# Performance work log

Hardware: AMD Instinct MI355X
Metric: run time of the kernel (lower is better)

The kernel has to match this reference:

```python
import jax, jax.numpy as jnp
import numpy as np

FEATURE_DIM = 256
TEMP = 0.1
BASE_TEMP = 0.07
MAX_SAMPLES = 1024
SIM_THR = 0.7


def setup_inputs() -> dict:
    key = jax.random.key(0)
    ks = jax.random.split(key, 8)
    B, C, H, W = 4, FEATURE_DIM, 160, 160
    s = 1.0 / np.sqrt(C)
    return {
        'feats': jax.random.normal(ks[0], (B, C, H, W), jnp.float32),
        'labels': jax.random.randint(ks[1], (B, H, W), 0, 2).astype(jnp.int64),
        'superpixel_indice': jax.random.randint(ks[2], (B, H, W), 0, 200).astype(jnp.int64),
        'w1': jax.random.normal(ks[3], (C, C), jnp.float32) * s,
        'b1': jnp.zeros((C,), jnp.float32),
        'w2': jax.random.normal(ks[4], (C, C), jnp.float32) * s,
        'b2': jnp.zeros((C,), jnp.float32),
        'wa1': jax.random.normal(ks[5], (64, C), jnp.float32) * s,
        'ba1': jnp.zeros((64,), jnp.float32),
        'wa2': jax.random.normal(ks[6], (1, 64), jnp.float32) * (1.0 / 8.0),
        'ba2': jnp.zeros((1,), jnp.float32),
    }


def _per_sample(f, w, lab, sp):
    # f: (N, C) normalized proj feats, w: (N,) pixel weights, lab/sp: (N,) int
    valid = lab == 1
    # deterministic sample: stable-sort valid pixels to the front, take MAX_SAMPLES
    order = jnp.argsort(jnp.where(valid, 0, 1).astype(jnp.int32))
    idx = order[:MAX_SAMPLES]
    sel = valid[idx]                       # (S,) real-sample mask (pads if <S valid)
    tf = f[idx]                            # (S, C)
    tw = w[idx]                            # (S,)
    ts = sp[idx]                           # (S,)
    sim = tf @ tf.T                        # (S, S)
    S = MAX_SAMPLES
    eye = jnp.eye(S, dtype=bool)
    pos = (ts[:, None] == ts[None, :]) & (sim > SIM_THR)
    pos = pos & sel[:, None] & sel[None, :] & ~eye
    exp_sim = jnp.exp(sim / TEMP) * sel[None, :].astype(sim.dtype)
    denom = exp_sim.sum(axis=1)            # (S,)
    log_prob = sim / TEMP - jnp.log(jnp.where(denom > 0, denom, 1.0))[:, None]
    pw = tw[:, None] * tw[None, :]
    pwm = jnp.where(pos, pw, 0.0)
    psum = pwm.sum()
    loss = -(TEMP / BASE_TEMP) * (pwm * jnp.where(pos, log_prob, 0.0)).sum() / jnp.where(psum > 0, psum, 1.0)
    has = psum > 0
    return jnp.where(has, loss, 0.0), has


def reference(feats, labels, superpixel_indice, w1, b1, w2, b2, wa1, ba1, wa2, ba2):
    B, C, H, W = feats.shape
    x = jnp.transpose(feats, (0, 2, 3, 1)).reshape(B, H * W, C)  # (B, N, C)
    proj = jax.nn.relu(x @ w1.T + b1) @ w2.T + b2                # 1x1 convs == per-pixel matmul
    attn = jax.nn.sigmoid(jax.nn.relu(x @ wa1.T + ba1) @ wa2.T + ba2)[..., 0]  # (B, N)
    nrm = jnp.linalg.norm(proj, axis=-1, keepdims=True)
    fn = proj / jnp.maximum(nrm, 1e-12)
    lab = labels.reshape(B, -1)
    sp = superpixel_indice.reshape(B, -1)
    losses, flags = jax.vmap(_per_sample)(fn, attn, lab, sp)
    n = flags.sum().astype(jnp.float32)
    return jnp.where(n > 0, losses.sum() / jnp.maximum(n, 1.0), 0.0)
```

## Files before the change

kernel.cpp:

```cpp
#include <hip/hip_runtime.h>
#include <hip/hip_bf16.h>
#include <math.h>

#define NPIX   25600
#define CDIM   256
#define SSEL   1024
#define BATCH  4
#define NCHUNK 25
#define INV_T  10.0f
#define RATIO  1.4285714285714286f
#define THR    0.7f

typedef __attribute__((ext_vector_type(8))) short bf16x8;
typedef __attribute__((ext_vector_type(4))) float f32x4;

__global__ __launch_bounds__(256) void pack_weights(
    const float* __restrict__ w1, const float* __restrict__ w2,
    const float* __restrict__ wa1, const int* __restrict__ labels,
    float* __restrict__ w1p, float* __restrict__ w2p, float* __restrict__ wa1p,
    float* __restrict__ denom, float* __restrict__ Prow, float* __restrict__ Ssum,
    int* __restrict__ counts) {
  int t = threadIdx.x;
  int e = blockIdx.x * 256 + t;
  if (e < 65536) {
    int kk = e & 3;
    int c  = (e >> 2) & 255;
    int k4 = e >> 10;
    int src = c * 256 + k4 * 4 + kk;
    w1p[e] = w1[src];
    w2p[e] = w2[src];
  }
  if (e < 16384) {
    int kk = e & 3;
    int c  = (e >> 2) & 63;
    int k4 = e >> 8;
    wa1p[e] = wa1[c * 256 + k4 * 4 + kk];
  }
  if (e < BATCH * SSEL) { denom[e] = 0.f; Prow[e] = 0.f; }
  if (e < BATCH) Ssum[e] = 0.f;

  if (blockIdx.x < BATCH * NCHUNK) {
    int b = blockIdx.x / NCHUNK, ch = blockIdx.x % NCHUNK;
    const int* lab = labels + b * NPIX + ch * 1024;
    int local = 0;
#pragma unroll
    for (int q = 0; q < 4; ++q) local += (lab[q * 256 + t] == 1);
    for (int off = 32; off > 0; off >>= 1) local += __shfl_xor(local, off, 64);
    __shared__ int ws[4];
    if ((t & 63) == 0) ws[t >> 6] = local;
    __syncthreads();
    if (t == 0) counts[blockIdx.x] = ws[0] + ws[1] + ws[2] + ws[3];
  }
}

__global__ __launch_bounds__(1024) void select_scatter(
    const int* __restrict__ labels, const int* __restrict__ sp,
    const int* __restrict__ counts,
    int* __restrict__ idx, int* __restrict__ selv, int* __restrict__ tsp) {
  int b = blockIdx.x / NCHUNK, ch = blockIdx.x % NCHUNK;
  int t = threadIdx.x;
  __shared__ int cs[NCHUNK];
  __shared__ int wave_tot[16];
  if (t < NCHUNK) cs[t] = counts[b * NCHUNK + t];
  __syncthreads();
  int Vtot = 0, vbase = 0;
#pragma unroll
  for (int c = 0; c < NCHUNK; ++c) {
    int v = cs[c];
    Vtot += v;
    if (c < ch) vbase += v;
  }
  int ibase = ch * 1024 - vbase;

  int i = ch * 1024 + t;
  int isv = (labels[b * NPIX + i] == 1) ? 1 : 0;
  int lane = t & 63, wid = t >> 6;
  unsigned long long mv = __ballot(isv);
  int pv = __popcll(mv & ((1ull << lane) - 1ull));
  if (lane == 0) wave_tot[wid] = __popcll(mv);
  __syncthreads();
  for (int w = 0; w < wid; ++w) pv += wave_tot[w];
  int gslot = isv ? (vbase + pv) : (Vtot + ibase + (t - pv));
  if (gslot < SSEL) {
    idx [b * SSEL + gslot] = i;
    selv[b * SSEL + gslot] = isv;
    tsp [b * SSEL + gslot] = sp[b * NPIX + i];
  }
}

#define RROWS 16
__global__ __launch_bounds__(256) void mlp_kernel(
    const float* __restrict__ feats,
    const float* __restrict__ w1p, const float* __restrict__ b1,
    const float* __restrict__ w2p, const float* __restrict__ b2,
    const float* __restrict__ wa1p, const float* __restrict__ ba1,
    const float* __restrict__ wa2, const float* __restrict__ ba2,
    const int* __restrict__ idx,
    unsigned short* __restrict__ fnh, unsigned short* __restrict__ fnl,
    float* __restrict__ tw) {
  int r0  = blockIdx.x * RROWS;
  int b   = r0 >> 10;
  int t   = threadIdx.x;
  int lane = t & 63;

  __shared__ float xs[RROWS][256];
  __shared__ float hs[RROWS][256];
  __shared__ float apart[RROWS][64];
  __shared__ float nrm[RROWS];
  __shared__ int   ridx[RROWS];

  if (t < RROWS) { ridx[t] = idx[r0 + t]; nrm[t] = 0.f; }
  __syncthreads();

  for (int e = t; e < RROWS * 256; e += 256) {
    int r = e & 15, c = e >> 4;
    xs[r][c] = feats[((long)b * CDIM + c) * NPIX + ridx[r]];
  }
  __syncthreads();

  const float4* xs4  = reinterpret_cast<const float4*>(&xs[0][0]);
  const float4* hs4  = reinterpret_cast<const float4*>(&hs[0][0]);
  const float4* w1p4 = reinterpret_cast<const float4*>(w1p);
  const float4* w2p4 = reinterpret_cast<const float4*>(w2p);
  const float4* wa1p4= reinterpret_cast<const float4*>(wa1p);

  {
    int ca = t & 63, rg = t >> 6;
    float aacc[4] = {0.f, 0.f, 0.f, 0.f};
#pragma unroll 2
    for (int k4 = 0; k4 < 64; ++k4) {
      float4 wv = wa1p4[k4 * 64 + ca];
#pragma unroll
      for (int r = 0; r < 4; ++r) {
        float4 xv = xs4[(rg * 4 + r) * 64 + k4];
        aacc[r] += xv.x * wv.x + xv.y * wv.y + xv.z * wv.z + xv.w * wv.w;
      }
    }
    float bb = ba1[ca], w2v = wa2[ca];
#pragma unroll
    for (int r = 0; r < 4; ++r)
      apart[rg * 4 + r][ca] = fmaxf(aacc[r] + bb, 0.f) * w2v;
  }

  int c  = t & 127;
  int rg = t >> 7;
  float acc[8][2];
#pragma unroll
  for (int r = 0; r < 8; ++r) { acc[r][0] = 0.f; acc[r][1] = 0.f; }
#pragma unroll 2
  for (int k4 = 0; k4 < 64; ++k4) {
    float4 w0 = w1p4[k4 * 256 + c];
    float4 w1v = w1p4[k4 * 256 + c + 128];
#pragma unroll
    for (int r = 0; r < 8; ++r) {
      float4 xv = xs4[(rg * 8 + r) * 64 + k4];
      acc[r][0] += xv.x * w0.x + xv.y * w0.y + xv.z * w0.z + xv.w * w0.w;
      acc[r][1] += xv.x * w1v.x + xv.y * w1v.y + xv.z * w1v.z + xv.w * w1v.w;
    }
  }
  {
    float bb0 = b1[c], bb1 = b1[c + 128];
#pragma unroll
    for (int r = 0; r < 8; ++r) {
      hs[rg * 8 + r][c]       = fmaxf(acc[r][0] + bb0, 0.f);
      hs[rg * 8 + r][c + 128] = fmaxf(acc[r][1] + bb1, 0.f);
    }
  }
  __syncthreads();

#pragma unroll
  for (int r = 0; r < 8; ++r) { acc[r][0] = 0.f; acc[r][1] = 0.f; }
#pragma unroll 2
  for (int k4 = 0; k4 < 64; ++k4) {
    float4 w0 = w2p4[k4 * 256 + c];
    float4 w1v = w2p4[k4 * 256 + c + 128];
#pragma unroll
    for (int r = 0; r < 8; ++r) {
      float4 xv = hs4[(rg * 8 + r) * 64 + k4];
      acc[r][0] += xv.x * w0.x + xv.y * w0.y + xv.z * w0.z + xv.w * w0.w;
      acc[r][1] += xv.x * w1v.x + xv.y * w1v.y + xv.z * w1v.z + xv.w * w1v.w;
    }
  }
  {
    float bb0 = b2[c], bb1 = b2[c + 128];
#pragma unroll
    for (int r = 0; r < 8; ++r) { acc[r][0] += bb0; acc[r][1] += bb1; }
  }

#pragma unroll
  for (int r = 0; r < 8; ++r) {
    float v = acc[r][0] * acc[r][0] + acc[r][1] * acc[r][1];
    for (int off = 32; off > 0; off >>= 1) v += __shfl_xor(v, off, 64);
    if (lane == 0) atomicAdd(&nrm[rg * 8 + r], v);
  }
  __syncthreads();
#pragma unroll
  for (int r = 0; r < 8; ++r) {
    float den = fmaxf(sqrtf(nrm[rg * 8 + r]), 1e-12f);
    long ro = (long)(r0 + rg * 8 + r) * CDIM;
    float v0 = acc[r][0] / den;
    float v1 = acc[r][1] / den;
    __hip_bfloat16 h0 = __float2bfloat16(v0);
    __hip_bfloat16 h1 = __float2bfloat16(v1);
    __hip_bfloat16 l0 = __float2bfloat16(v0 - __bfloat162float(h0));
    __hip_bfloat16 l1 = __float2bfloat16(v1 - __bfloat162float(h1));
    fnh[ro + c]       = *reinterpret_cast<unsigned short*>(&h0);
    fnh[ro + c + 128] = *reinterpret_cast<unsigned short*>(&h1);
    fnl[ro + c]       = *reinterpret_cast<unsigned short*>(&l0);
    fnl[ro + c + 128] = *reinterpret_cast<unsigned short*>(&l1);
  }

  if (t < RROWS) {
    float s = ba2[0];
    for (int c2 = 0; c2 < 64; ++c2) s += apart[t][c2];
    tw[r0 + t] = 1.f / (1.f + expf(-s));
  }
}

__global__ __launch_bounds__(256) void sim_kernel(
    const unsigned short* __restrict__ fnh, const unsigned short* __restrict__ fnl,
    const float* __restrict__ tw,
    const int* __restrict__ selv, const int* __restrict__ tsp,
    float* __restrict__ denom, float* __restrict__ Prow, float* __restrict__ Ssum) {
  int b = blockIdx.y;
  int t = threadIdx.x;
  int lane = t & 63, w = t >> 6;
  int m = lane & 15, q = lane >> 4;

  int rem = blockIdx.x, ti = 0;
  while (rem >= (16 - ti)) { rem -= (16 - ti); ++ti; }
  int tj = ti + rem;
  bool diag = (ti == tj);
  int i0 = ti * 64, j0 = tj * 64;
  int base = b << 10;

  __shared__ __align__(16) unsigned short Ah[64 * 72], Al[64 * 72];
  __shared__ __align__(16) unsigned short Bhh[64 * 72], Bll[64 * 72];
  __shared__ float drl[64], Prl[64];
  __shared__ float dclw[4][64], Pclw[4][64];
  __shared__ float swv[4];

  const unsigned short* Bh = diag ? Ah : Bhh;
  const unsigned short* Bl = diag ? Al : Bll;

  f32x4 acc[4];
#pragma unroll
  for (int nt = 0; nt < 4; ++nt) acc[nt] = {0.f, 0.f, 0.f, 0.f};

  for (int kk = 0; kk < 4; ++kk) {
    __syncthreads();
#pragma unroll
    for (int p = 0; p < 2; ++p) {
      int e = p * 256 + t;
      int row = e >> 3, kg = e & 7;
      int lo = row * 72 + kg * 8;
      int gi_ = (base + i0 + row) * 256 + kk * 64 + kg * 8;
      *(uint4*)&Ah[lo] = *(const uint4*)&fnh[gi_];
      *(uint4*)&Al[lo] = *(const uint4*)&fnl[gi_];
      if (!diag) {
        int gj_ = (base + j0 + row) * 256 + kk * 64 + kg * 8;
        *(uint4*)&Bhh[lo] = *(const uint4*)&fnh[gj_];
        *(uint4*)&Bll[lo] = *(const uint4*)&fnl[gj_];
      }
    }
    __syncthreads();
#pragma unroll
    for (int ks = 0; ks < 2; ++ks) {
      int koff = ks * 32 + q * 8;
      int arow = w * 16 + m;
      bf16x8 ah = *(const bf16x8*)&Ah[arow * 72 + koff];
      bf16x8 al = *(const bf16x8*)&Al[arow * 72 + koff];
#pragma unroll
      for (int nt = 0; nt < 4; ++nt) {
        bf16x8 bh = *(const bf16x8*)&Bh[(nt * 16 + m) * 72 + koff];
        bf16x8 bl = *(const bf16x8*)&Bl[(nt * 16 + m) * 72 + koff];
        acc[nt] = __builtin_amdgcn_mfma_f32_16x16x32_bf16(ah, bh, acc[nt], 0, 0, 0);
        acc[nt] = __builtin_amdgcn_mfma_f32_16x16x32_bf16(ah, bl, acc[nt], 0, 0, 0);
        acc[nt] = __builtin_amdgcn_mfma_f32_16x16x32_bf16(al, bh, acc[nt], 0, 0, 0);
      }
    }
  }

  int   gi[4], gj[4], si[4], sj[4], ci[4], cj[4];
  float twi[4], twj[4];
#pragma unroll
  for (int reg = 0; reg < 4; ++reg) {
    int i = i0 + w * 16 + q * 4 + reg;
    gi[reg] = i; twi[reg] = tw[base + i];
    si[reg] = selv[base + i]; ci[reg] = tsp[base + i];
  }
#pragma unroll
  for (int nt = 0; nt < 4; ++nt) {
    int j = j0 + nt * 16 + m;
    gj[nt] = j; twj[nt] = tw[base + j];
    sj[nt] = selv[base + j]; cj[nt] = tsp[base + j];
  }

  float dR[4] = {0, 0, 0, 0}, PR[4] = {0, 0, 0, 0};
  float dC[4] = {0, 0, 0, 0}, PC[4] = {0, 0, 0, 0};
  float Sp = 0.f;
#pragma unroll
  for (int nt = 0; nt < 4; ++nt) {
#pragma unroll
    for (int reg = 0; reg < 4; ++reg) {
      float s = acc[nt][reg];
      float e10 = __expf(s * INV_T);
      if (sj[nt]) dR[reg] += e10;
      if (si[reg]) dC[nt] += e10;
      if (si[reg] && sj[nt] && (ci[reg] == cj[nt]) && (s > THR) && (gi[reg] != gj[nt])) {
        float pw = twi[reg] * twj[nt];
        PR[reg] += pw;
        PC[nt] += pw;
        Sp += pw * s;
      }
    }
  }

  for (int off = 8; off > 0; off >>= 1) {
#pragma unroll
    for (int reg = 0; reg < 4; ++reg) {
      dR[reg] += __shfl_xor(dR[reg], off, 64);
      PR[reg] += __shfl_xor(PR[reg], off, 64);
    }
  }
  if (m == 0) {
#pragma unroll
    for (int reg = 0; reg < 4; ++reg) {
      drl[w * 16 + q * 4 + reg] = dR[reg];
      Prl[w * 16 + q * 4 + reg] = PR[reg];
    }
  }
  if (!diag) {
    for (int off = 32; off >= 16; off >>= 1) {
#pragma unroll
      for (int nt = 0; nt < 4; ++nt) {
        dC[nt] += __shfl_xor(dC[nt], off, 64);
        PC[nt] += __shfl_xor(PC[nt], off, 64);
      }
    }
    if (q == 0) {
#pragma unroll
      for (int nt = 0; nt < 4; ++nt) {
        dclw[w][nt * 16 + m] = dC[nt];
        Pclw[w][nt * 16 + m] = PC[nt];
      }
    }
  }
  for (int off = 32; off > 0; off >>= 1) Sp += __shfl_xor(Sp, off, 64);
  if (lane == 0) swv[w] = Sp;
  __syncthreads();

  if (t < 64) {
    atomicAdd(&denom[base + i0 + t], drl[t]);
    atomicAdd(&Prow [base + i0 + t], Prl[t]);
    if (!diag) {
      float dc = dclw[0][t] + dclw[1][t] + dclw[2][t] + dclw[3][t];
      float pc = Pclw[0][t] + Pclw[1][t] + Pclw[2][t] + Pclw[3][t];
      atomicAdd(&denom[base + j0 + t], dc);
      atomicAdd(&Prow [base + j0 + t], pc);
    }
  }
  if (t == 0) {
    float St = swv[0] + swv[1] + swv[2] + swv[3];
    atomicAdd(&Ssum[b], diag ? St : 2.f * St);
  }
}

__global__ __launch_bounds__(1024) void finalize_kernel(
    const float* __restrict__ denom, const float* __restrict__ Prow,
    const float* __restrict__ Ssum, float* __restrict__ out) {
  int t = threadIdx.x;
  int b = t >> 8, u = t & 255;
  float P = 0.f, L = 0.f;
#pragma unroll
  for (int q = 0; q < 4; ++q) {
    int s = u + q * 256;
    float p = Prow[b * SSEL + s];
    float D = denom[b * SSEL + s];
    P += p;
    L += p * logf(D > 0.f ? D : 1.f);
  }
  for (int off = 32; off > 0; off >>= 1) {
    P += __shfl_xor(P, off, 64);
    L += __shfl_xor(L, off, 64);
  }
  __shared__ float wP[16], wL[16];
  int lane = t & 63, w = t >> 6;
  if (lane == 0) { wP[w] = P; wL[w] = L; }
  __syncthreads();
  if (t == 0) {
    float total = 0.f, n = 0.f;
    for (int bb = 0; bb < BATCH; ++bb) {
      float psum = wP[4 * bb] + wP[4 * bb + 1] + wP[4 * bb + 2] + wP[4 * bb + 3];
      float lsum = wL[4 * bb] + wL[4 * bb + 1] + wL[4 * bb + 2] + wL[4 * bb + 3];
      if (psum > 0.f) {
        float wls = Ssum[bb] * INV_T - lsum;
        total += -RATIO * wls / psum;
        n += 1.f;
      }
    }
    out[0] = (n > 0.f) ? (total / n) : 0.f;
  }
}

extern "C" void kernel_launch(void* const* d_in, const int* in_sizes, int n_in,
                              void* d_out, int out_size, void* d_ws, size_t ws_size,
                              hipStream_t stream) {
  const float* feats = (const float*)d_in[0];
  const int*   labels = (const int*)d_in[1];
  const int*   sp     = (const int*)d_in[2];
  const float* w1  = (const float*)d_in[3];
  const float* b1  = (const float*)d_in[4];
  const float* w2  = (const float*)d_in[5];
  const float* b2  = (const float*)d_in[6];
  const float* wa1 = (const float*)d_in[7];
  const float* ba1 = (const float*)d_in[8];
  const float* wa2 = (const float*)d_in[9];
  const float* ba2 = (const float*)d_in[10];
  float* out = (float*)d_out;

  float* W    = (float*)d_ws;
  float* w1p  = W;
  float* w2p  = w1p  + 65536;
  float* wa1p = w2p  + 65536;
  unsigned short* fnh = (unsigned short*)(wa1p + 16384);
  unsigned short* fnl = fnh + 1048576;
  float* tw   = (float*)(fnl + 1048576);
  float* denom= tw   + 4096;
  float* Prow = denom+ 4096;
  float* Ssum = Prow + 4096;
  int*   idx  = (int*)(Ssum + 4);
  int*   selv = idx  + 4096;
  int*   tsp  = selv + 4096;
  int*   counts = tsp + 4096;

  pack_weights<<<256, 256, 0, stream>>>(w1, w2, wa1, labels, w1p, w2p, wa1p,
                                        denom, Prow, Ssum, counts);
  select_scatter<<<BATCH * NCHUNK, 1024, 0, stream>>>(labels, sp, counts,
                                                      idx, selv, tsp);
  mlp_kernel<<<(BATCH * SSEL) / RROWS, 256, 0, stream>>>(
      feats, w1p, b1, w2p, b2, wa1p, ba1, wa2, ba2, idx, fnh, fnl, tw);
  sim_kernel<<<dim3(136, BATCH), 256, 0, stream>>>(fnh, fnl, tw, selv, tsp,
                                                   denom, Prow, Ssum);
  finalize_kernel<<<1, 1024, 0, stream>>>(denom, Prow, Ssum, out);
}
```

Before: 222.4 us.

## Remap MLP thread tiling so each thread owns two rows and eight columns

Reorganizes the per-row MLP in mlp_kernel so each thread computes 2 rows by 8 strided columns instead of 8 rows by 2 columns. Shared-memory activation reads become broadcasts within a 32-lane group, while each weight float4 is reused across two rows. The row norm is now reduced with a 32-lane shuffle and written directly, with no shared atomics. Weight global loads per thread rise relative to LDS reads, which may raise L2 traffic.

```diff
diff --git a/kernel.cpp b/kernel.cpp
--- a/kernel.cpp
+++ b/kernel.cpp
@@ -101,7 +101,6 @@
   int r0  = blockIdx.x * RROWS;
   int b   = r0 >> 10;
   int t   = threadIdx.x;
-  int lane = t & 63;
 
   __shared__ float xs[RROWS][256];
   __shared__ float hs[RROWS][256];
@@ -109,7 +108,7 @@
   __shared__ float nrm[RROWS];
   __shared__ int   ridx[RROWS];
 
-  if (t < RROWS) { ridx[t] = idx[r0 + t]; nrm[t] = 0.f; }
+  if (t < RROWS) ridx[t] = idx[r0 + t];
   __syncthreads();
 
   for (int e = t; e < RROWS * 256; e += 256) {
@@ -125,89 +124,101 @@
   const float4* wa1p4= reinterpret_cast<const float4*>(wa1p);
 
   {
-    int ca = t & 63, rg = t >> 6;
+    int ca = t & 15, r = t >> 4;
     float aacc[4] = {0.f, 0.f, 0.f, 0.f};
 #pragma unroll 2
     for (int k4 = 0; k4 < 64; ++k4) {
-      float4 wv = wa1p4[k4 * 64 + ca];
-#pragma unroll
-      for (int r = 0; r < 4; ++r) {
-        float4 xv = xs4[(rg * 4 + r) * 64 + k4];
-        aacc[r] += xv.x * wv.x + xv.y * wv.y + xv.z * wv.z + xv.w * wv.w;
-      }
-    }
-    float bb = ba1[ca], w2v = wa2[ca];
-#pragma unroll
-    for (int r = 0; r < 4; ++r)
-      apart[rg * 4 + r][ca] = fmaxf(aacc[r] + bb, 0.f) * w2v;
-  }
-
-  int c  = t & 127;
-  int rg = t >> 7;
-  float acc[8][2];
-#pragma unroll
-  for (int r = 0; r < 8; ++r) { acc[r][0] = 0.f; acc[r][1] = 0.f; }
+      float4 xv = xs4[r * 64 + k4];
+#pragma unroll
+      for (int j = 0; j < 4; ++j) {
+        float4 wv = wa1p4[k4 * 64 + ca + 16 * j];
+        aacc[j] += xv.x * wv.x + xv.y * wv.y + xv.z * wv.z + xv.w * wv.w;
+      }
+    }
+#pragma unroll
+    for (int j = 0; j < 4; ++j) {
+      int cc = ca + 16 * j;
+      apart[r][cc] = fmaxf(aacc[j] + ba1[cc], 0.f) * wa2[cc];
+    }
+  }
+
+  int c  = t & 31;
+  int p  = t >> 5;
+  int ra = 2 * p, rb = 2 * p + 1;
+  float acc0[8], acc1[8];
+#pragma unroll
+  for (int j = 0; j < 8; ++j) { acc0[j] = 0.f; acc1[j] = 0.f; }
 #pragma unroll 2
   for (int k4 = 0; k4 < 64; ++k4) {
-    float4 w0 = w1p4[k4 * 256 + c];
-    float4 w1v = w1p4[k4 * 256 + c + 128];
-#pragma unroll
-    for (int r = 0; r < 8; ++r) {
-      float4 xv = xs4[(rg * 8 + r) * 64 + k4];
-      acc[r][0] += xv.x * w0.x + xv.y * w0.y + xv.z * w0.z + xv.w * w0.w;
-      acc[r][1] += xv.x * w1v.x + xv.y * w1v.y + xv.z * w1v.z + xv.w * w1v.w;
-    }
-  }
-  {
-    float bb0 = b1[c], bb1 = b1[c + 128];
-#pragma unroll
-    for (int r = 0; r < 8; ++r) {
-      hs[rg * 8 + r][c]       = fmaxf(acc[r][0] + bb0, 0.f);
-      hs[rg * 8 + r][c + 128] = fmaxf(acc[r][1] + bb1, 0.f);
-    }
-  }
-  __syncthreads();
-
-#pragma unroll
-  for (int r = 0; r < 8; ++r) { acc[r][0] = 0.f; acc[r][1] = 0.f; }
+    float4 xa = xs4[ra * 64 + k4];
+    float4 xb = xs4[rb * 64 + k4];
+#pragma unroll
+    for (int j = 0; j < 8; ++j) {
+      float4 wv = w1p4[k4 * 256 + c + 32 * j];
+      acc0[j] += xa.x * wv.x + xa.y * wv.y + xa.z * wv.z + xa.w * wv.w;
+      acc1[j] += xb.x * wv.x + xb.y * wv.y + xb.z * wv.z + xb.w * wv.w;
+    }
+  }
+#pragma unroll
+  for (int j = 0; j < 8; ++j) {
+    int cc = c + 32 * j;
+    float bb = b1[cc];
+    hs[ra][cc] = fmaxf(acc0[j] + bb, 0.f);
+    hs[rb][cc] = fmaxf(acc1[j] + bb, 0.f);
+  }
+  __syncthreads();
+
+#pragma unroll
+  for (int j = 0; j < 8; ++j) { acc0[j] = 0.f; acc1[j] = 0.f; }
 #pragma unroll 2
   for (int k4 = 0; k4 < 64; ++k4) {
-    float4 w0 = w2p4[k4 * 256 + c];
-    float4 w1v = w2p4[k4 * 256 + c + 128];
-#pragma unroll
-    for (int r = 0; r < 8; ++r) {
-      float4 xv = hs4[(rg * 8 + r) * 64 + k4];
-      acc[r][0] += xv.x * w0.x + xv.y * w0.y + xv.z * w0.z + xv.w * w0.w;
-      acc[r][1] += xv.x * w1v.x + xv.y * w1v.y + xv.z * w1v.z + xv.w * w1v.w;
-    }
-  }
+    float4 xa = hs4[ra * 64 + k4];
+    float4 xb = hs4[rb * 64 + k4];
+#pragma unroll
+    for (int j = 0; j < 8; ++j) {
+      float4 wv = w2p4[k4 * 256 + c + 32 * j];
+      acc0[j] += xa.x * wv.x + xa.y * wv.y + xa.z * wv.z + xa.w * wv.w;
+      acc1[j] += xb.x * wv.x + xb.y * wv.y + xb.z * wv.z + xb.w * wv.w;
+    }
+  }
+#pragma unroll
+  for (int j = 0; j < 8; ++j) {
+    int cc = c + 32 * j;
+    float bb = b2[cc];
+    acc0[j] += bb;
+    acc1[j] += bb;
+  }
+
   {
-    float bb0 = b2[c], bb1 = b2[c + 128];
-#pragma unroll
-    for (int r = 0; r < 8; ++r) { acc[r][0] += bb0; acc[r][1] += bb1; }
-  }
-
-#pragma unroll
-  for (int r = 0; r < 8; ++r) {
-    float v = acc[r][0] * acc[r][0] + acc[r][1] * acc[r][1];
-    for (int off = 32; off > 0; off >>= 1) v += __shfl_xor(v, off, 64);
-    if (lane == 0) atomicAdd(&nrm[rg * 8 + r], v);
-  }
-  __syncthreads();
-#pragma unroll
-  for (int r = 0; r < 8; ++r) {
-    float den = fmaxf(sqrtf(nrm[rg * 8 + r]), 1e-12f);
-    long ro = (long)(r0 + rg * 8 + r) * CDIM;
-    float v0 = acc[r][0] / den;
-    float v1 = acc[r][1] / den;
-    __hip_bfloat16 h0 = __float2bfloat16(v0);
-    __hip_bfloat16 h1 = __float2bfloat16(v1);
-    __hip_bfloat16 l0 = __float2bfloat16(v0 - __bfloat162float(h0));
-    __hip_bfloat16 l1 = __float2bfloat16(v1 - __bfloat162float(h1));
-    fnh[ro + c]       = *reinterpret_cast<unsigned short*>(&h0);
-    fnh[ro + c + 128] = *reinterpret_cast<unsigned short*>(&h1);
-    fnl[ro + c]       = *reinterpret_cast<unsigned short*>(&l0);
-    fnl[ro + c + 128] = *reinterpret_cast<unsigned short*>(&l1);
+    float v0 = 0.f, v1 = 0.f;
+#pragma unroll
+    for (int j = 0; j < 8; ++j) { v0 += acc0[j] * acc0[j]; v1 += acc1[j] * acc1[j]; }
+    for (int off = 16; off > 0; off >>= 1) {
+      v0 += __shfl_xor(v0, off, 64);
+      v1 += __shfl_xor(v1, off, 64);
+    }
+    if ((t & 31) == 0) { nrm[ra] = v0; nrm[rb] = v1; }
+  }
+  __syncthreads();
+  {
+    float dena = fmaxf(sqrtf(nrm[ra]), 1e-12f);
+    float denb = fmaxf(sqrtf(nrm[rb]), 1e-12f);
+    long roa = (long)(r0 + ra) * CDIM;
+    long rob = (long)(r0 + rb) * CDIM;
+#pragma unroll
+    for (int j = 0; j < 8; ++j) {
+      int cc = c + 32 * j;
+      float va = acc0[j] / dena;
+      float vb = acc1[j] / denb;
+      __hip_bfloat16 ha = __float2bfloat16(va);
+      __hip_bfloat16 hb = __float2bfloat16(vb);
+      __hip_bfloat16 la = __float2bfloat16(va - __bfloat162float(ha));
+      __hip_bfloat16 lb = __float2bfloat16(vb - __bfloat162float(hb));
+      fnh[roa + cc] = *reinterpret_cast<unsigned short*>(&ha);
+      fnh[rob + cc] = *reinterpret_cast<unsigned short*>(&hb);
+      fnl[roa + cc] = *reinterpret_cast<unsigned short*>(&la);
+      fnl[rob + cc] = *reinterpret_cast<unsigned short*>(&lb);
+    }
   }
 
   if (t < RROWS) {
```

Result: slower. 232.1 us (+4.4%).

## Move projection MLP onto bf16x3 MFMA GEMMs split across several kernels

Applied to the files above, without the earlier changes.

Replaces the fused FP32 SIMT MLP kernel with a pipeline of kernels. A gather/cast kernel splits the selected features into bf16 hi/lo parts. Two MFMA GEMM kernels then use a three-product bf16 split to approximate FP32 accuracy, with the attention head folded into the first GEMM grid. A separate normalize/split kernel finishes the step. The aim is to cut the FP32 FMA cost of the 4096x256x256 matmuls, at the price of extra launches and intermediate buffers round-tripping through global memory.

```diff
diff --git a/kernel.cpp b/kernel.cpp
--- a/kernel.cpp
+++ b/kernel.cpp
@@ -13,30 +13,31 @@
 
 typedef __attribute__((ext_vector_type(8))) short bf16x8;
 typedef __attribute__((ext_vector_type(4))) float f32x4;
+typedef unsigned short u16;
+
+__device__ __forceinline__ void bf16_split(float v, u16& h, u16& l) {
+  __hip_bfloat16 hb = __float2bfloat16(v);
+  __hip_bfloat16 lb = __float2bfloat16(v - __bfloat162float(hb));
+  h = *reinterpret_cast<u16*>(&hb);
+  l = *reinterpret_cast<u16*>(&lb);
+}
 
 __global__ __launch_bounds__(256) void pack_weights(
     const float* __restrict__ w1, const float* __restrict__ w2,
     const float* __restrict__ wa1, const int* __restrict__ labels,
-    float* __restrict__ w1p, float* __restrict__ w2p, float* __restrict__ wa1p,
+    u16* __restrict__ w1hb, u16* __restrict__ w1lb,
+    u16* __restrict__ w2hb, u16* __restrict__ w2lb,
+    u16* __restrict__ wahb, u16* __restrict__ walb,
     float* __restrict__ denom, float* __restrict__ Prow, float* __restrict__ Ssum,
-    int* __restrict__ counts) {
+    float* __restrict__ nrm, int* __restrict__ counts) {
   int t = threadIdx.x;
   int e = blockIdx.x * 256 + t;
   if (e < 65536) {
-    int kk = e & 3;
-    int c  = (e >> 2) & 255;
-    int k4 = e >> 10;
-    int src = c * 256 + k4 * 4 + kk;
-    w1p[e] = w1[src];
-    w2p[e] = w2[src];
-  }
-  if (e < 16384) {
-    int kk = e & 3;
-    int c  = (e >> 2) & 63;
-    int k4 = e >> 8;
-    wa1p[e] = wa1[c * 256 + k4 * 4 + kk];
-  }
-  if (e < BATCH * SSEL) { denom[e] = 0.f; Prow[e] = 0.f; }
+    bf16_split(w1[e], w1hb[e], w1lb[e]);
+    bf16_split(w2[e], w2hb[e], w2lb[e]);
+  }
+  if (e < 16384) bf16_split(wa1[e], wahb[e], walb[e]);
+  if (e < BATCH * SSEL) { denom[e] = 0.f; Prow[e] = 0.f; nrm[e] = 0.f; }
   if (e < BATCH) Ssum[e] = 0.f;
 
   if (blockIdx.x < BATCH * NCHUNK) {
@@ -44,7 +45,7 @@
     const int* lab = labels + b * NPIX + ch * 1024;
     int local = 0;
 #pragma unroll
-    for (int q = 0; q < 4; ++q) local += (lab[q * 256 + t] == 1);
+    for (int qq = 0; qq < 4; ++qq) local += (lab[qq * 256 + t] == 1);
     for (int off = 32; off > 0; off >>= 1) local += __shfl_xor(local, off, 64);
     __shared__ int ws[4];
     if ((t & 63) == 0) ws[t >> 6] = local;
@@ -88,137 +89,215 @@
   }
 }
 
-#define RROWS 16
-__global__ __launch_bounds__(256) void mlp_kernel(
-    const float* __restrict__ feats,
-    const float* __restrict__ w1p, const float* __restrict__ b1,
-    const float* __restrict__ w2p, const float* __restrict__ b2,
-    const float* __restrict__ wa1p, const float* __restrict__ ba1,
+__global__ __launch_bounds__(256) void gather_cast(
+    const float* __restrict__ feats, const int* __restrict__ idx,
+    u16* __restrict__ xh, u16* __restrict__ xl) {
+  int r0 = blockIdx.x * 16;
+  int b  = r0 >> 10;
+  int t  = threadIdx.x;
+  __shared__ int ridx[16];
+  if (t < 16) ridx[t] = idx[r0 + t];
+  __syncthreads();
+  const float* fb = feats + ((long)b * CDIM + t) * NPIX;
+#pragma unroll 4
+  for (int r = 0; r < 16; ++r) {
+    float v = fb[ridx[r]];
+    u16 h, l;
+    bf16_split(v, h, l);
+    long o = (long)(r0 + r) * CDIM + t;
+    xh[o] = h;
+    xl[o] = l;
+  }
+}
+
+__global__ __launch_bounds__(256) void gemm1_kernel(
+    const u16* __restrict__ xh, const u16* __restrict__ xl,
+    const u16* __restrict__ w1hb, const u16* __restrict__ w1lb,
+    const u16* __restrict__ wahb, const u16* __restrict__ walb,
+    const float* __restrict__ b1, const float* __restrict__ ba1,
     const float* __restrict__ wa2, const float* __restrict__ ba2,
-    const int* __restrict__ idx,
-    unsigned short* __restrict__ fnh, unsigned short* __restrict__ fnl,
-    float* __restrict__ tw) {
-  int r0  = blockIdx.x * RROWS;
-  int b   = r0 >> 10;
-  int t   = threadIdx.x;
-  int lane = t & 63;
-
-  __shared__ float xs[RROWS][256];
-  __shared__ float hs[RROWS][256];
-  __shared__ float apart[RROWS][64];
-  __shared__ float nrm[RROWS];
-  __shared__ int   ridx[RROWS];
-
-  if (t < RROWS) { ridx[t] = idx[r0 + t]; nrm[t] = 0.f; }
-  __syncthreads();
-
-  for (int e = t; e < RROWS * 256; e += 256) {
-    int r = e & 15, c = e >> 4;
-    xs[r][c] = feats[((long)b * CDIM + c) * NPIX + ridx[r]];
-  }
-  __syncthreads();
-
-  const float4* xs4  = reinterpret_cast<const float4*>(&xs[0][0]);
-  const float4* hs4  = reinterpret_cast<const float4*>(&hs[0][0]);
-  const float4* w1p4 = reinterpret_cast<const float4*>(w1p);
-  const float4* w2p4 = reinterpret_cast<const float4*>(w2p);
-  const float4* wa1p4= reinterpret_cast<const float4*>(wa1p);
-
-  {
-    int ca = t & 63, rg = t >> 6;
-    float aacc[4] = {0.f, 0.f, 0.f, 0.f};
-#pragma unroll 2
-    for (int k4 = 0; k4 < 64; ++k4) {
-      float4 wv = wa1p4[k4 * 64 + ca];
-#pragma unroll
-      for (int r = 0; r < 4; ++r) {
-        float4 xv = xs4[(rg * 4 + r) * 64 + k4];
-        aacc[r] += xv.x * wv.x + xv.y * wv.y + xv.z * wv.z + xv.w * wv.w;
-      }
-    }
-    float bb = ba1[ca], w2v = wa2[ca];
-#pragma unroll
-    for (int r = 0; r < 4; ++r)
-      apart[rg * 4 + r][ca] = fmaxf(aacc[r] + bb, 0.f) * w2v;
-  }
-
-  int c  = t & 127;
-  int rg = t >> 7;
-  float acc[8][2];
-#pragma unroll
-  for (int r = 0; r < 8; ++r) { acc[r][0] = 0.f; acc[r][1] = 0.f; }
-#pragma unroll 2
-  for (int k4 = 0; k4 < 64; ++k4) {
-    float4 w0 = w1p4[k4 * 256 + c];
-    float4 w1v = w1p4[k4 * 256 + c + 128];
-#pragma unroll
-    for (int r = 0; r < 8; ++r) {
-      float4 xv = xs4[(rg * 8 + r) * 64 + k4];
-      acc[r][0] += xv.x * w0.x + xv.y * w0.y + xv.z * w0.z + xv.w * w0.w;
-      acc[r][1] += xv.x * w1v.x + xv.y * w1v.y + xv.z * w1v.z + xv.w * w1v.w;
-    }
-  }
-  {
-    float bb0 = b1[c], bb1 = b1[c + 128];
-#pragma unroll
-    for (int r = 0; r < 8; ++r) {
-      hs[rg * 8 + r][c]       = fmaxf(acc[r][0] + bb0, 0.f);
-      hs[rg * 8 + r][c + 128] = fmaxf(acc[r][1] + bb1, 0.f);
-    }
-  }
-  __syncthreads();
-
-#pragma unroll
-  for (int r = 0; r < 8; ++r) { acc[r][0] = 0.f; acc[r][1] = 0.f; }
-#pragma unroll 2
-  for (int k4 = 0; k4 < 64; ++k4) {
-    float4 w0 = w2p4[k4 * 256 + c];
-    float4 w1v = w2p4[k4 * 256 + c + 128];
-#pragma unroll
-    for (int r = 0; r < 8; ++r) {
-      float4 xv = hs4[(rg * 8 + r) * 64 + k4];
-      acc[r][0] += xv.x * w0.x + xv.y * w0.y + xv.z * w0.z + xv.w * w0.w;
-      acc[r][1] += xv.x * w1v.x + xv.y * w1v.y + xv.z * w1v.z + xv.w * w1v.w;
-    }
-  }
-  {
-    float bb0 = b2[c], bb1 = b2[c + 128];
-#pragma unroll
-    for (int r = 0; r < 8; ++r) { acc[r][0] += bb0; acc[r][1] += bb1; }
-  }
-
-#pragma unroll
-  for (int r = 0; r < 8; ++r) {
-    float v = acc[r][0] * acc[r][0] + acc[r][1] * acc[r][1];
-    for (int off = 32; off > 0; off >>= 1) v += __shfl_xor(v, off, 64);
-    if (lane == 0) atomicAdd(&nrm[rg * 8 + r], v);
-  }
-  __syncthreads();
-#pragma unroll
-  for (int r = 0; r < 8; ++r) {
-    float den = fmaxf(sqrtf(nrm[rg * 8 + r]), 1e-12f);
-    long ro = (long)(r0 + rg * 8 + r) * CDIM;
-    float v0 = acc[r][0] / den;
-    float v1 = acc[r][1] / den;
-    __hip_bfloat16 h0 = __float2bfloat16(v0);
-    __hip_bfloat16 h1 = __float2bfloat16(v1);
-    __hip_bfloat16 l0 = __float2bfloat16(v0 - __bfloat162float(h0));
-    __hip_bfloat16 l1 = __float2bfloat16(v1 - __bfloat162float(h1));
-    fnh[ro + c]       = *reinterpret_cast<unsigned short*>(&h0);
-    fnh[ro + c + 128] = *reinterpret_cast<unsigned short*>(&h1);
-    fnl[ro + c]       = *reinterpret_cast<unsigned short*>(&l0);
-    fnl[ro + c + 128] = *reinterpret_cast<unsigned short*>(&l1);
-  }
-
-  if (t < RROWS) {
-    float s = ba2[0];
-    for (int c2 = 0; c2 < 64; ++c2) s += apart[t][c2];
-    tw[r0 + t] = 1.f / (1.f + expf(-s));
-  }
+    u16* __restrict__ hh, u16* __restrict__ hl, float* __restrict__ tw) {
+  int n  = blockIdx.x;
+  int i0 = blockIdx.y * 64;
+  int t = threadIdx.x;
+  int lane = t & 63, w = t >> 6, m = lane & 15, q = lane >> 4;
+  bool attn = (n == 4);
+  const u16* bsh = attn ? wahb : (w1hb + n * 64 * 256);
+  const u16* bsl = attn ? walb : (w1lb + n * 64 * 256);
+
+  __shared__ __align__(16) u16 Ah[64 * 72], Al[64 * 72];
+  __shared__ __align__(16) u16 Bh[64 * 72], Bl[64 * 72];
+
+  f32x4 acc[4];
+#pragma unroll
+  for (int nt = 0; nt < 4; ++nt) acc[nt] = {0.f, 0.f, 0.f, 0.f};
+
+  for (int kk = 0; kk < 4; ++kk) {
+    __syncthreads();
+#pragma unroll
+    for (int p = 0; p < 2; ++p) {
+      int e = p * 256 + t;
+      int row = e >> 3, kg = e & 7;
+      int lo = row * 72 + kg * 8;
+      int go = row * 256 + kk * 64 + kg * 8;
+      *(uint4*)&Ah[lo] = *(const uint4*)&xh[(i0 + row) * 256 + kk * 64 + kg * 8];
+      *(uint4*)&Al[lo] = *(const uint4*)&xl[(i0 + row) * 256 + kk * 64 + kg * 8];
+      *(uint4*)&Bh[lo] = *(const uint4*)&bsh[go];
+      *(uint4*)&Bl[lo] = *(const uint4*)&bsl[go];
+    }
+    __syncthreads();
+#pragma unroll
+    for (int ks = 0; ks < 2; ++ks) {
+      int koff = ks * 32 + q * 8;
+      bf16x8 ah = *(const bf16x8*)&Ah[(w * 16 + m) * 72 + koff];
+      bf16x8 al = *(const bf16x8*)&Al[(w * 16 + m) * 72 + koff];
+#pragma unroll
+      for (int nt = 0; nt < 4; ++nt) {
+        bf16x8 bh = *(const bf16x8*)&Bh[(nt * 16 + m) * 72 + koff];
+        bf16x8 bl = *(const bf16x8*)&Bl[(nt * 16 + m) * 72 + koff];
+        acc[nt] = __builtin_amdgcn_mfma_f32_16x16x32_bf16(ah, bh, acc[nt], 0, 0, 0);
+        acc[nt] = __builtin_amdgcn_mfma_f32_16x16x32_bf16(ah, bl, acc[nt], 0, 0, 0);
+        acc[nt] = __builtin_amdgcn_mfma_f32_16x16x32_bf16(al, bh, acc[nt], 0, 0, 0);
+      }
+    }
+  }
+
+  if (!attn) {
+#pragma unroll
+    for (int nt = 0; nt < 4; ++nt) {
+      int col = n * 64 + nt * 16 + m;
+      float bb = b1[col];
+#pragma unroll
+      for (int reg = 0; reg < 4; ++reg) {
+        int row = i0 + w * 16 + q * 4 + reg;
+        float v = fmaxf(acc[nt][reg] + bb, 0.f);
+        u16 h, l;
+        bf16_split(v, h, l);
+        hh[row * 256 + col] = h;
+        hl[row * 256 + col] = l;
+      }
+    }
+  } else {
+    float part[4] = {0.f, 0.f, 0.f, 0.f};
+#pragma unroll
+    for (int nt = 0; nt < 4; ++nt) {
+      int ca = nt * 16 + m;
+      float bb = ba1[ca], wv = wa2[ca];
+#pragma unroll
+      for (int reg = 0; reg < 4; ++reg)
+        part[reg] += fmaxf(acc[nt][reg] + bb, 0.f) * wv;
+    }
+    for (int off = 8; off > 0; off >>= 1) {
+#pragma unroll
+      for (int reg = 0; reg < 4; ++reg)
+        part[reg] += __shfl_xor(part[reg], off, 64);
+    }
+    if (m == 0) {
+      float bb2 = ba2[0];
+#pragma unroll
+      for (int reg = 0; reg < 4; ++reg) {
+        int row = i0 + w * 16 + q * 4 + reg;
+        tw[row] = 1.f / (1.f + expf(-(part[reg] + bb2)));
+      }
+    }
+  }
+}
+
+__global__ __launch_bounds__(256) void gemm2_kernel(
+    const u16* __restrict__ hh, const u16* __restrict__ hl,
+    const u16* __restrict__ w2hb, const u16* __restrict__ w2lb,
+    const float* __restrict__ b2,
+    float* __restrict__ pbuf, float* __restrict__ nrm) {
+  int n  = blockIdx.x;
+  int i0 = blockIdx.y * 64;
+  int t = threadIdx.x;
+  int lane = t & 63, w = t >> 6, m = lane & 15, q = lane >> 4;
+  const u16* bsh = w2hb + n * 64 * 256;
+  const u16* bsl = w2lb + n * 64 * 256;
+
+  __shared__ __align__(16) u16 Ah[64 * 72], Al[64 * 72];
+  __shared__ __align__(16) u16 Bh[64 * 72], Bl[64 * 72];
+
+  f32x4 acc[4];
+#pragma unroll
+  for (int nt = 0; nt < 4; ++nt) acc[nt] = {0.f, 0.f, 0.f, 0.f};
+
+  for (int kk = 0; kk < 4; ++kk) {
+    __syncthreads();
+#pragma unroll
+    for (int p = 0; p < 2; ++p) {
+      int e = p * 256 + t;
+      int row = e >> 3, kg = e & 7;
+      int lo = row * 72 + kg * 8;
+      int go = row * 256 + kk * 64 + kg * 8;
+      *(uint4*)&Ah[lo] = *(const uint4*)&hh[(i0 + row) * 256 + kk * 64 + kg * 8];
+      *(uint4*)&Al[lo] = *(const uint4*)&hl[(i0 + row) * 256 + kk * 64 + kg * 8];
+      *(uint4*)&Bh[lo] = *(const uint4*)&bsh[go];
+      *(uint4*)&Bl[lo] = *(const uint4*)&bsl[go];
+    }
+    __syncthreads();
+#pragma unroll
+    for (int ks = 0; ks < 2; ++ks) {
+      int koff = ks * 32 + q * 8;
+      bf16x8 ah = *(const bf16x8*)&Ah[(w * 16 + m) * 72 + koff];
+      bf16x8 al = *(const bf16x8*)&Al[(w * 16 + m) * 72 + koff];
+#pragma unroll
+      for (int nt = 0; nt < 4; ++nt) {
+        bf16x8 bh = *(const bf16x8*)&Bh[(nt * 16 + m) * 72 + koff];
+        bf16x8 bl = *(const bf16x8*)&Bl[(nt * 16 + m) * 72 + koff];
+        acc[nt] = __builtin_amdgcn_mfma_f32_16x16x32_bf16(ah, bh, acc[nt], 0, 0, 0);
+        acc[nt] = __builtin_amdgcn_mfma_f32_16x16x32_bf16(ah, bl, acc[nt], 0, 0, 0);
+        acc[nt] = __builtin_amdgcn_mfma_f32_16x16x32_bf16(al, bh, acc[nt], 0, 0, 0);
+      }
+    }
+  }
+
+  float part[4] = {0.f, 0.f, 0.f, 0.f};
+#pragma unroll
+  for (int nt = 0; nt < 4; ++nt) {
+    int col = n * 64 + nt * 16 + m;
+    float bb = b2[col];
+#pragma unroll
+    for (int reg = 0; reg < 4; ++reg) {
+      int row = i0 + w * 16 + q * 4 + reg;
+      float p = acc[nt][reg] + bb;
+      pbuf[row * 256 + col] = p;
+      part[reg] += p * p;
+    }
+  }
+  for (int off = 8; off > 0; off >>= 1) {
+#pragma unroll
+    for (int reg = 0; reg < 4; ++reg)
+      part[reg] += __shfl_xor(part[reg], off, 64);
+  }
+  if (m == 0) {
+#pragma unroll
+    for (int reg = 0; reg < 4; ++reg) {
+      int row = i0 + w * 16 + q * 4 + reg;
+      atomicAdd(&nrm[row], part[reg]);
+    }
+  }
+}
+
+__global__ __launch_bounds__(256) void norm_split(
+    const float* __restrict__ pbuf, const float* __restrict__ nrm,
+    u16* __restrict__ fnh, u16* __restrict__ fnl) {
+  int e = blockIdx.x * 256 + threadIdx.x;
+  long base = (long)e * 8;
+  int row = e >> 5;
+  float inv = 1.f / fmaxf(sqrtf(nrm[row]), 1e-12f);
+  float4 pa = *(const float4*)&pbuf[base];
+  float4 pb = *(const float4*)&pbuf[base + 4];
+  float v[8] = {pa.x, pa.y, pa.z, pa.w, pb.x, pb.y, pb.z, pb.w};
+  u16 hs[8], ls[8];
+#pragma unroll
+  for (int j = 0; j < 8; ++j) bf16_split(v[j] * inv, hs[j], ls[j]);
+  *(uint4*)&fnh[base] = *(const uint4*)hs;
+  *(uint4*)&fnl[base] = *(const uint4*)ls;
 }
 
 __global__ __launch_bounds__(256) void sim_kernel(
-    const unsigned short* __restrict__ fnh, const unsigned short* __restrict__ fnl,
+    const u16* __restrict__ fnh, const u16* __restrict__ fnl,
     const float* __restrict__ tw,
     const int* __restrict__ selv, const int* __restrict__ tsp,
     float* __restrict__ denom, float* __restrict__ Prow, float* __restrict__ Ssum) {
@@ -234,14 +313,14 @@
   int i0 = ti * 64, j0 = tj * 64;
   int base = b << 10;
 
-  __shared__ __align__(16) unsigned short Ah[64 * 72], Al[64 * 72];
-  __shared__ __align__(16) unsigned short Bhh[64 * 72], Bll[64 * 72];
+  __shared__ __align__(16) u16 Ah[64 * 72], Al[64 * 72];
+  __shared__ __align__(16) u16 Bhh[64 * 72], Bll[64 * 72];
   __shared__ float drl[64], Prl[64];
   __shared__ float dclw[4][64], Pclw[4][64];
   __shared__ float swv[4];
 
-  const unsigned short* Bh = diag ? Ah : Bhh;
-  const unsigned short* Bl = diag ? Al : Bll;
+  const u16* Bh = diag ? Ah : Bhh;
+  const u16* Bl = diag ? Al : Bll;
 
   f32x4 acc[4];
 #pragma unroll
@@ -419,27 +498,41 @@
   const float* ba2 = (const float*)d_in[10];
   float* out = (float*)d_out;
 
-  float* W    = (float*)d_ws;
-  float* w1p  = W;
-  float* w2p  = w1p  + 65536;
-  float* wa1p = w2p  + 65536;
-  unsigned short* fnh = (unsigned short*)(wa1p + 16384);
-  unsigned short* fnl = fnh + 1048576;
-  float* tw   = (float*)(fnl + 1048576);
-  float* denom= tw   + 4096;
-  float* Prow = denom+ 4096;
-  float* Ssum = Prow + 4096;
-  int*   idx  = (int*)(Ssum + 4);
-  int*   selv = idx  + 4096;
-  int*   tsp  = selv + 4096;
-  int*   counts = tsp + 4096;
-
-  pack_weights<<<256, 256, 0, stream>>>(w1, w2, wa1, labels, w1p, w2p, wa1p,
-                                        denom, Prow, Ssum, counts);
+  char* W = (char*)d_ws;
+  u16* w1hb = (u16*)W;               W += 65536 * 2;
+  u16* w1lb = (u16*)W;               W += 65536 * 2;
+  u16* w2hb = (u16*)W;               W += 65536 * 2;
+  u16* w2lb = (u16*)W;               W += 65536 * 2;
+  u16* wahb = (u16*)W;               W += 16384 * 2;
+  u16* walb = (u16*)W;               W += 16384 * 2;
+  u16* xh   = (u16*)W;               W += 1048576 * 2;
+  u16* xl   = (u16*)W;               W += 1048576 * 2;
+  u16* hh   = (u16*)W;               W += 1048576 * 2;
+  u16* hl   = (u16*)W;               W += 1048576 * 2;
+  u16* fnh  = (u16*)W;               W += 1048576 * 2;
+  u16* fnl  = (u16*)W;               W += 1048576 * 2;
+  float* pbuf = (float*)W;           W += 1048576 * 4;
+  float* nrm  = (float*)W;           W += 4096 * 4;
+  float* tw   = (float*)W;           W += 4096 * 4;
+  float* denom= (float*)W;           W += 4096 * 4;
+  float* Prow = (float*)W;           W += 4096 * 4;
+  float* Ssum = (float*)W;           W += 4 * 4;
+  int*   idx  = (int*)W;             W += 4096 * 4;
+  int*   selv = (int*)W;             W += 4096 * 4;
+  int*   tsp  = (int*)W;             W += 4096 * 4;
+  int*   counts = (int*)W;           W += 128 * 4;
+
+  pack_weights<<<256, 256, 0, stream>>>(w1, w2, wa1, labels,
+                                        w1hb, w1lb, w2hb, w2lb, wahb, walb,
+                                        denom, Prow, Ssum, nrm, counts);
   select_scatter<<<BATCH * NCHUNK, 1024, 0, stream>>>(labels, sp, counts,
                                                       idx, selv, tsp);
-  mlp_kernel<<<(BATCH * SSEL) / RROWS, 256, 0, stream>>>(
-      feats, w1p, b1, w2p, b2, wa1p, ba1, wa2, ba2, idx, fnh, fnl, tw);
+  gather_cast<<<256, 256, 0, stream>>>(feats, idx, xh, xl);
+  gemm1_kernel<<<dim3(5, 64), 256, 0, stream>>>(xh, xl, w1hb, w1lb, wahb, walb,
+                                                b1, ba1, wa2, ba2, hh, hl, tw);
+  gemm2_kernel<<<dim3(4, 64), 256, 0, stream>>>(hh, hl, w2hb, w2lb, b2,
+                                                pbuf, nrm);
+  norm_split<<<512, 256, 0, stream>>>(pbuf, nrm, fnh, fnl);
   sim_kernel<<<dim3(136, BATCH), 256, 0, stream>>>(fnh, fnl, tw, selv, tsp,
                                                    denom, Prow, Ssum);
   finalize_kernel<<<1, 1024, 0, stream>>>(denom, Prow, Ssum, out);
```

Result: faster. 195.8 us (-12.0%).
